# Kernel tuning notes

Hardware: AMD Instinct MI355X
Metric: run time of the kernel (lower is better)

The kernel has to match this reference:

```python
import jax, jax.numpy as jnp
import numpy as np

D_MODEL = 2048
HEADS = 16
INNER = 8192
SEQ = 2048
BATCH = 1  # source code's mask.reshape(B,1,L,L) requires B==1
EPS = 1e-5


def _layer_norm(x, gamma, beta):
    mu = jnp.mean(x, axis=-1, keepdims=True)
    var = jnp.mean(jnp.square(x - mu), axis=-1, keepdims=True)
    return (x - mu) * jax.lax.rsqrt(var + EPS) * gamma + beta


def setup_inputs() -> dict:
    key = jax.random.key(0)
    ks = jax.random.split(key, 14)
    s = 0.02
    return {
        "x": jax.random.normal(ks[0], (BATCH, SEQ, D_MODEL), jnp.float32),
        # weights stored as (in, out)
        "Wqkv": jax.random.normal(ks[1], (D_MODEL, 3 * D_MODEL), jnp.float32) * s,
        "bqkv": jnp.zeros((3 * D_MODEL,), jnp.float32),
        "Wo": jax.random.normal(ks[2], (D_MODEL, D_MODEL), jnp.float32) * s,
        "bo": jnp.zeros((D_MODEL,), jnp.float32),
        "W1": jax.random.normal(ks[3], (D_MODEL, INNER), jnp.float32) * s,
        "b1": jnp.zeros((INNER,), jnp.float32),
        "W2": jax.random.normal(ks[4], (INNER, D_MODEL), jnp.float32) * s,
        "b2": jnp.zeros((D_MODEL,), jnp.float32),
        "g1": jnp.ones((D_MODEL,), jnp.float32),
        "be1": jnp.zeros((D_MODEL,), jnp.float32),
        "g2": jnp.ones((D_MODEL,), jnp.float32),
        "be2": jnp.zeros((D_MODEL,), jnp.float32),
    }


def reference(x, Wqkv, bqkv, Wo, bo, W1, b1, W2, b2, g1, be1, g2, be2):
    B, L, D = x.shape
    H, hd = HEADS, D // HEADS
    qkv = x @ Wqkv + bqkv                       # [B,L,3D]
    q, k, v = jnp.split(qkv, 3, axis=-1)
    q = q.reshape(B, L, H, hd)
    k = k.reshape(B, L, H, hd)
    v = v.reshape(B, L, H, hd)
    # NOTE: faithful to source, scale is 1/sqrt(D) not 1/sqrt(head_dim)
    scores = jnp.einsum("bqhd,bkhd->bhqk", q, k) / jnp.sqrt(jnp.float32(D))
    causal = jnp.tril(jnp.ones((L, L), bool))   # [L,L] broadcast over B,H
    scores = jnp.where(causal, scores, -jnp.inf)
    attn = jax.nn.softmax(scores, axis=-1)      # dropout = identity (eval)
    out = jnp.einsum("bhqk,bkhd->bqhd", attn, v).reshape(B, L, D)
    lin = out @ Wo + bo
    h = _layer_norm(x + lin, g1, be1)
    ff = jax.nn.gelu(h @ W1 + b1, approximate=False) @ W2 + b2
    return _layer_norm(h + ff, g2, be2)
```

## Files before the change

kernel.cpp:

```cpp
#include <hip/hip_runtime.h>
#include <hip/hip_bf16.h>

typedef unsigned short u16;
typedef __attribute__((ext_vector_type(8))) short frag8;
typedef __attribute__((ext_vector_type(4))) float facc4;

#define L_SEQ 2048
#define D_MODEL 2048
#define N_HEADS 16
#define HEAD_D 128
#define N_QKV 6144
#define D_INNER 8192

__device__ __forceinline__ u16 f2b(float f) {
    __hip_bfloat16 h = __float2bfloat16(f);
    return *reinterpret_cast<u16*>(&h);
}

__device__ __forceinline__ float b2f(u16 u) {
    __hip_bfloat16 h = *reinterpret_cast<__hip_bfloat16*>(&u);
    return __bfloat162float(h);
}

__device__ __forceinline__ void gload_lds16(const void* g, void* l) {
    __builtin_amdgcn_global_load_lds(
        (const __attribute__((address_space(1))) unsigned int*)g,
        (__attribute__((address_space(3))) unsigned int*)l, 16, 0, 0);
}

__device__ __forceinline__ float gelu_exact(float x) {
    return 0.5f * x * (1.0f + erff(x * 0.7071067811865475f));
}

__global__ __launch_bounds__(256) void cvt_bf16_kernel(const float* __restrict__ in, u16* __restrict__ out, int n) {
    const int i = (blockIdx.x * 256 + threadIdx.x) * 8;
    if (i >= n) return;
    float4 a = *(const float4*)(in + i);
    float4 b = *(const float4*)(in + i + 4);
    u16 tmp[8];
    tmp[0] = f2b(a.x); tmp[1] = f2b(a.y); tmp[2] = f2b(a.z); tmp[3] = f2b(a.w);
    tmp[4] = f2b(b.x); tmp[5] = f2b(b.y); tmp[6] = f2b(b.z); tmp[7] = f2b(b.w);
    *(uint4*)(out + i) = *(uint4*)tmp;
}

__global__ __launch_bounds__(256) void tr_cvt64(const float* __restrict__ in, u16* __restrict__ out, int R, int C) {
    __shared__ float t[64][68];
    const int bx = blockIdx.x * 64;
    const int by = blockIdx.y * 64;
    const int tid = threadIdx.x;
    {
        const int r = tid >> 2;
        const int c4 = (tid & 3) * 16;
        const float* src = in + (size_t)(by + r) * C + bx + c4;
#pragma unroll
        for (int j = 0; j < 4; ++j)
            *(float4*)&t[r][c4 + 4 * j] = *(const float4*)(src + 4 * j);
    }
    __syncthreads();
    {
        const int cc = tid >> 2;
        const int rr0 = (tid & 3) * 16;
        u16 tmp[16];
#pragma unroll
        for (int j = 0; j < 16; ++j) tmp[j] = f2b(t[rr0 + j][cc]);
        u16* dst = out + (size_t)(bx + cc) * R + by + rr0;
        *(uint4*)(dst) = *(uint4*)&tmp[0];
        *(uint4*)(dst + 8) = *(uint4*)&tmp[8];
    }
}

template <int EPI>
__global__ __launch_bounds__(512, 2) void gemm256(const u16* __restrict__ A, const u16* __restrict__ Bt,
                                                  const float* __restrict__ bias, void* __restrict__ Cout,
                                                  u16* __restrict__ q0, u16* __restrict__ q1,
                                                  u16* __restrict__ q2, u16* __restrict__ q3,
                                                  int M, int N, int K, int kseg, int nbm) {
    __shared__ u16 lds[2 * 32768];
    const int tid = threadIdx.x;
    const int lane = tid & 63, wid = tid >> 6;
    const int wm = wid >> 2, wn = wid & 3;
    const int l15 = lane & 15, g4 = lane >> 4;

    const int nwg = gridDim.x;
    const int q8 = nwg >> 3;
    const int wg = (blockIdx.x & 7) * q8 + (blockIdx.x >> 3);
    const int bm = wg % nbm, bn = wg / nbm;
    const int kb = blockIdx.z * kseg;
    const int ksz = (blockIdx.z == (int)gridDim.z - 1) ? (K - kb) : kseg;
    const int nt = ksz >> 6;

    const int rr = tid >> 3;
    const int kk8 = tid & 7;
    const int srcE = (kk8 ^ (rr & 7)) << 3;
    const u16* aS = A + (size_t)(bm * 256 + rr) * K + kb + srcE;
    const u16* bS = Bt + (size_t)(bn * 256 + ((rr >> 5) << 6) + (rr & 31)) * K + kb + srcE;
    const size_t r128 = (size_t)128 * K;
    const size_t r64 = (size_t)64 * K;
    const size_t c32 = (size_t)32 * K;

    auto stA = [&](int tt, int h) {
        u16* d = &lds[((tt & 1) << 15) + (h << 13)];
        const u16* g = aS + (size_t)tt * 64 + (h ? r64 : 0);
        gload_lds16(g, d + tid * 8);
        gload_lds16(g + r128, d + 4096 + tid * 8);
    };
    auto stB = [&](int tt, int h) {
        u16* d = &lds[((tt & 1) << 15) + 16384 + (h << 13)];
        const u16* g = bS + (size_t)tt * 64 + (h ? c32 : 0);
        gload_lds16(g, d + tid * 8);
        gload_lds16(g + r128, d + 4096 + tid * 8);
    };

    const int ch0 = (g4 ^ (l15 & 7)) << 3;
    const int ch1 = ch0 ^ 32;
    const int aRdBase = (wm * 64 + l15) * 64;
    const int bRdBase = (wn * 32 + l15) * 64;

    frag8 a[4][2], b0[2][2], b1[2][2];
    facc4 acc[8][4] = {};

    auto rdA = [&](int bufo, int mh) {
#pragma unroll
        for (int mi = 0; mi < 4; ++mi) {
            const int base = bufo + mh * 8192 + aRdBase + mi * 1024;
            a[mi][0] = *(const frag8*)&lds[base + ch0];
            a[mi][1] = *(const frag8*)&lds[base + ch1];
        }
    };
    auto rdB = [&](int bufo, int nh, frag8(&bb)[2][2]) {
#pragma unroll
        for (int ni = 0; ni < 2; ++ni) {
            const int base = bufo + 16384 + nh * 8192 + bRdBase + ni * 1024;
            bb[ni][0] = *(const frag8*)&lds[base + ch0];
            bb[ni][1] = *(const frag8*)&lds[base + ch1];
        }
    };
    auto quad = [&](int mh, int nh, frag8(&bb)[2][2]) {
        __builtin_amdgcn_s_setprio(1);
#pragma unroll
        for (int kh = 0; kh < 2; ++kh)
#pragma unroll
            for (int mi = 0; mi < 4; ++mi)
#pragma unroll
                for (int ni = 0; ni < 2; ++ni)
                    acc[mh * 4 + mi][nh * 2 + ni] =
                        __builtin_amdgcn_mfma_f32_16x16x32_bf16(a[mi][kh], bb[ni][kh],
                                                                acc[mh * 4 + mi][nh * 2 + ni], 0, 0, 0);
        __builtin_amdgcn_s_setprio(0);
    };

#define SB __builtin_amdgcn_sched_barrier(0)
#define BAR __builtin_amdgcn_s_barrier()

    stA(0, 0); stB(0, 0); stB(0, 1); stA(0, 1);
    if (nt > 1) { stA(1, 0); stB(1, 0); stB(1, 1); }
    if (nt > 2) asm volatile("s_waitcnt vmcnt(6)" ::: "memory");
    else        asm volatile("s_waitcnt vmcnt(0)" ::: "memory");
    BAR; SB;

    for (int t = 0; t < nt; ++t) {
        const int bufo = (t & 1) << 15;
        rdA(bufo, 0);
        rdB(bufo, 0, b0);
        if (t + 1 < nt) stA(t + 1, 1);
        SB; BAR; SB;
        quad(0, 0, b0);
        BAR; SB;
        rdB(bufo, 1, b1);
        if (t + 2 < nt) stA(t + 2, 0);
        SB; BAR; SB;
        quad(0, 1, b1);
        BAR; SB;
        rdA(bufo, 1);
        if (t + 2 < nt) stB(t + 2, 0);
        SB; BAR; SB;
        quad(1, 0, b0);
        BAR; SB;
        if (t + 2 < nt) stB(t + 2, 1);
        SB; BAR; SB;
        quad(1, 1, b1);
        if (t + 2 < nt) asm volatile("s_waitcnt vmcnt(6)" ::: "memory");
        else            asm volatile("s_waitcnt vmcnt(0)" ::: "memory");
        BAR; SB;
    }
#undef SB
#undef BAR

    const int row0 = bm * 256 + wm * 128 + g4 * 4;
    const int col0 = bn * 256 + wn * 64 + l15;
    u16* pout = nullptr;
    if (EPI == 3) {
        const int z = blockIdx.z;
        pout = (z == 0) ? q0 : (z == 1) ? q1 : (z == 2) ? q2 : q3;
    }
#pragma unroll
    for (int nf = 0; nf < 4; nf++) {
        const int col = col0 + nf * 16;
        const float bv = (EPI == 3) ? 0.0f : bias[col];
#pragma unroll
        for (int mf = 0; mf < 8; mf++) {
#pragma unroll
            for (int r = 0; r < 4; r++) {
                const int row = row0 + mf * 16 + r;
                float v = acc[mf][nf][r] + bv;
                if (EPI == 2) v = gelu_exact(v);
                if (EPI == 0)
                    ((float*)Cout)[(size_t)row * N + col] = v;
                else if (EPI == 3)
                    pout[(size_t)row * N + col] = f2b(v);
                else
                    ((u16*)Cout)[(size_t)row * N + col] = f2b(v);
            }
        }
    }
}

__global__ __launch_bounds__(256) void attn_kernel(const u16* __restrict__ qkv,
                                                   float* __restrict__ O0, float* __restrict__ O1,
                                                   float* __restrict__ ml) {
    __shared__ u16 kT[2][64 * 128];
    __shared__ u16 vT[2][128 * 64];
    const int h = blockIdx.y;
    const int z = blockIdx.z;
    const int qb = (blockIdx.y < 8) ? 31 - (int)blockIdx.x : (int)blockIdx.x;
    const int tid = threadIdx.x;
    const int lane = tid & 63, w = tid >> 6;
    const int l15 = lane & 15, g4 = lane >> 4;
    const int q0 = qb * 64 + w * 16;
    const float scale = 0.022097086912079608f;

    const int ntt = qb + 1;
    const int hsp = (ntt + 1) >> 1;
    const int t0 = z ? hsp : 0;
    const int t1 = z ? ntt : hsp;

    frag8 qf[4];
    {
        const u16* qrow = qkv + (size_t)(q0 + l15) * N_QKV + h * HEAD_D + g4 * 8;
#pragma unroll
        for (int c = 0; c < 4; c++) qf[c] = *(const frag8*)(qrow + c * 32);
    }

    float m_run = -1e30f, l_run = 0.0f;
    facc4 o[8] = {};

    const int src0 = ((g4 & 1) << 5) + l15;
    const int src1 = src0 + 16;
    const bool hi = (g4 & 2) != 0;

    auto stageK = [&](int kbase, int buf) {
        const u16* kg_ptr = qkv + (size_t)kbase * N_QKV + D_MODEL + h * HEAD_D;
#pragma unroll
        for (int p = 0; p < 4; ++p) {
            const int c = p * 256 + tid;
            const int row = c >> 4;
            const int colb = (c & 15) << 4;
            const int srcb = colb ^ ((row & 7) << 4);
            gload_lds16(kg_ptr + (size_t)row * N_QKV + (srcb >> 1), &kT[buf][c * 8]);
        }
    };
    auto loadV = [&](int kbase, uint4 (&vv)[4]) {
        const u16* vg_ptr = qkv + (size_t)kbase * N_QKV + 2 * D_MODEL + h * HEAD_D;
#pragma unroll
        for (int i = 0; i < 4; ++i)
            vv[i] = *(const uint4*)(vg_ptr + (size_t)lane * N_QKV + w * 32 + i * 8);
    };
    auto writeV = [&](const uint4 (&vv)[4], int buf) {
#pragma unroll
        for (int i = 0; i < 4; ++i) {
            const u16* pv = (const u16*)&vv[i];
#pragma unroll
            for (int e = 0; e < 8; ++e) {
                const int d = w * 32 + i * 8 + e;
                vT[buf][d * 64 + ((((lane >> 3) ^ (d & 7)) << 3) | (lane & 7))] = pv[e];
            }
        }
    };

    if (t0 < t1) {
        uint4 vv[4];
        stageK(t0 * 64, 0);
        loadV(t0 * 64, vv);
        writeV(vv, 0);
    }
    __syncthreads();

    for (int t = t0; t < t1; ++t) {
        const int buf = (t - t0) & 1;
        const int kbase = t * 64;
        const bool last = (t == t1 - 1);

        uint4 vv[4];
        if (!last) {
            stageK(kbase + 64, buf ^ 1);
            loadV(kbase + 64, vv);
        }

        if (kbase <= q0 + 15) {
            const u16* kTb = kT[buf];
            const u16* vTb = vT[buf];
            float st[16];
            float mx = -1e30f;
#pragma unroll
            for (int ks = 0; ks < 4; ++ks) {
                const int k0 = kbase + ks * 16;
                if (k0 <= q0 + 15) {
                    facc4 s = {};
                    const int kl = ks * 16 + l15;
#pragma unroll
                    for (int c = 0; c < 4; ++c) {
                        const int colb = (g4 * 16 + c * 64) ^ ((kl & 7) << 4);
                        frag8 kf = *(const frag8*)&kTb[kl * 128 + (colb >> 1)];
                        s = __builtin_amdgcn_mfma_f32_16x16x32_bf16(kf, qf[c], s, 0, 0, 0);
                    }
#pragma unroll
                    for (int r = 0; r < 4; ++r) {
                        float v = s[r] * scale;
                        const int key = k0 + g4 * 4 + r;
                        if (key > q0 + l15) v = -1e30f;
                        st[ks * 4 + r] = v;
                        mx = fmaxf(mx, v);
                    }
                } else {
#pragma unroll
                    for (int r = 0; r < 4; ++r) st[ks * 4 + r] = -1e30f;
                }
            }

            mx = fmaxf(mx, __shfl_xor(mx, 16));
            mx = fmaxf(mx, __shfl_xor(mx, 32));
            const bool skip = __all(mx <= m_run + 8.0f);
            const float m_new = skip ? m_run : fmaxf(m_run, mx);
            const float alpha = __expf(m_run - m_new);
            float ps = 0.0f;
            uint2 pb[4];
#pragma unroll
            for (int ks = 0; ks < 4; ++ks) {
                const float p0 = __expf(st[ks * 4 + 0] - m_new);
                const float p1 = __expf(st[ks * 4 + 1] - m_new);
                const float p2 = __expf(st[ks * 4 + 2] - m_new);
                const float p3 = __expf(st[ks * 4 + 3] - m_new);
                ps += (p0 + p1) + (p2 + p3);
                pb[ks].x = (unsigned)f2b(p0) | ((unsigned)f2b(p1) << 16);
                pb[ks].y = (unsigned)f2b(p2) | ((unsigned)f2b(p3) << 16);
            }
            ps += __shfl_xor(ps, 16);
            ps += __shfl_xor(ps, 32);
            l_run = l_run * alpha + ps;
            m_run = m_new;
            if (!skip) {
#pragma unroll
                for (int c8 = 0; c8 < 8; ++c8)
#pragma unroll
                    for (int r = 0; r < 4; ++r) o[c8][r] *= alpha;
            }

#pragma unroll
            for (int kp = 0; kp < 2; ++kp) {
                if (kbase + kp * 32 <= q0 + 15) {
                    const uint2 a = pb[2 * kp], b = pb[2 * kp + 1];
                    const unsigned a0 = __shfl(a.x, src0), a1 = __shfl(a.y, src0);
                    const unsigned a2 = __shfl(a.x, src1), a3 = __shfl(a.y, src1);
                    const unsigned b0 = __shfl(b.x, src0), b1 = __shfl(b.y, src0);
                    const unsigned b2 = __shfl(b.x, src1), b3 = __shfl(b.y, src1);
                    union { unsigned u[4]; frag8 f; } pu;
                    pu.u[0] = hi ? b0 : a0;
                    pu.u[1] = hi ? b1 : a1;
                    pu.u[2] = hi ? b2 : a2;
                    pu.u[3] = hi ? b3 : a3;
                    const frag8 pf = pu.f;
#pragma unroll
                    for (int c8 = 0; c8 < 8; ++c8) {
                        const int d = c8 * 16 + l15;
                        const int ch = (((kp * 4 + g4) ^ (l15 & 7)) << 3);
                        frag8 vf = *(const frag8*)&vTb[d * 64 + ch];
                        o[c8] = __builtin_amdgcn_mfma_f32_16x16x32_bf16(vf, pf, o[c8], 0, 0, 0);
                    }
                }
            }
        }

        if (!last) writeV(vv, buf ^ 1);
        __syncthreads();
    }

    const int row = q0 + l15;
    if (g4 == 0) {
        const size_t mlo = (((size_t)z * N_HEADS + h) * L_SEQ + row) * 2;
        ml[mlo + 0] = m_run;
        ml[mlo + 1] = l_run;
    }
    if (t0 < t1) {
        float* Op = z ? O1 : O0;
        float* orow = Op + (size_t)row * D_MODEL + h * HEAD_D;
#pragma unroll
        for (int c8 = 0; c8 < 8; ++c8)
            *(facc4*)&orow[c8 * 16 + g4 * 4] = o[c8];
    }
}

__global__ __launch_bounds__(256) void attn_combine(const float* __restrict__ O0, const float* __restrict__ O1,
                                                    const float* __restrict__ ml, u16* __restrict__ out) {
    const int row = blockIdx.x;
    const int tid = threadIdx.x;
    const size_t rb = (size_t)row * D_MODEL;
#pragma unroll
    for (int i = 0; i < 8; ++i) {
        const int c = tid + i * 256;
        const int h = c >> 7;
        const size_t o0 = (((size_t)0 * N_HEADS + h) * L_SEQ + row) * 2;
        const size_t o1 = (((size_t)1 * N_HEADS + h) * L_SEQ + row) * 2;
        const float m0 = ml[o0 + 0], l0 = ml[o0 + 1];
        const float m1 = ml[o1 + 0], l1 = ml[o1 + 1];
        float v;
        if (l1 > 0.0f) {
            const float m = fmaxf(m0, m1);
            const float w0 = __expf(m0 - m);
            const float w1 = __expf(m1 - m);
            v = (O0[rb + c] * w0 + O1[rb + c] * w1) / (l0 * w0 + l1 * w1);
        } else {
            v = O0[rb + c] / l0;
        }
        out[rb + c] = f2b(v);
    }
}

__global__ __launch_bounds__(256) void ln1_part_kernel(const float* __restrict__ x,
                                                       const u16* __restrict__ p0, const u16* __restrict__ p1,
                                                       const u16* __restrict__ p2, const u16* __restrict__ p3,
                                                       const float* __restrict__ bias,
                                                       const float* __restrict__ gamma, const float* __restrict__ beta,
                                                       u16* __restrict__ outb) {
    __shared__ float red[8];
    const int row = blockIdx.x;
    const int tid = threadIdx.x;
    const size_t rb = (size_t)row * D_MODEL;
    float v[8];
    float s = 0.0f, s2 = 0.0f;
#pragma unroll
    for (int i = 0; i < 8; i++) {
        const int c = tid + i * 256;
        float xv = x[rb + c] + bias[c] +
                   b2f(p0[rb + c]) + b2f(p1[rb + c]) + b2f(p2[rb + c]) + b2f(p3[rb + c]);
        v[i] = xv;
        s += xv;
        s2 += xv * xv;
    }
#pragma unroll
    for (int off = 32; off; off >>= 1) {
        s += __shfl_xor(s, off);
        s2 += __shfl_xor(s2, off);
    }
    if ((tid & 63) == 0) { red[(tid >> 6) * 2] = s; red[(tid >> 6) * 2 + 1] = s2; }
    __syncthreads();
    s = red[0] + red[2] + red[4] + red[6];
    s2 = red[1] + red[3] + red[5] + red[7];
    const float mean = s * (1.0f / D_MODEL);
    const float var = s2 * (1.0f / D_MODEL) - mean * mean;
    const float rstd = rsqrtf(var + 1e-5f);
#pragma unroll
    for (int i = 0; i < 8; i++) {
        const int c = tid + i * 256;
        outb[rb + c] = f2b((v[i] - mean) * rstd * gamma[c] + beta[c]);
    }
}

__global__ __launch_bounds__(256) void ln_part_kernel(const u16* __restrict__ hb,
                                                      const u16* __restrict__ p0, const u16* __restrict__ p1,
                                                      const u16* __restrict__ p2, const u16* __restrict__ p3,
                                                      const float* __restrict__ bias,
                                                      const float* __restrict__ gamma, const float* __restrict__ beta,
                                                      float* __restrict__ outf) {
    __shared__ float red[8];
    const int row = blockIdx.x;
    const int tid = threadIdx.x;
    const size_t rb = (size_t)row * D_MODEL;
    float v[8];
    float s = 0.0f, s2 = 0.0f;
#pragma unroll
    for (int i = 0; i < 8; i++) {
        const int c = tid + i * 256;
        float x = b2f(hb[rb + c]) + bias[c] +
                  b2f(p0[rb + c]) + b2f(p1[rb + c]) + b2f(p2[rb + c]) + b2f(p3[rb + c]);
        v[i] = x;
        s += x;
        s2 += x * x;
    }
#pragma unroll
    for (int off = 32; off; off >>= 1) {
        s += __shfl_xor(s, off);
        s2 += __shfl_xor(s2, off);
    }
    if ((tid & 63) == 0) { red[(tid >> 6) * 2] = s; red[(tid >> 6) * 2 + 1] = s2; }
    __syncthreads();
    s = red[0] + red[2] + red[4] + red[6];
    s2 = red[1] + red[3] + red[5] + red[7];
    const float mean = s * (1.0f / D_MODEL);
    const float var = s2 * (1.0f / D_MODEL) - mean * mean;
    const float rstd = rsqrtf(var + 1e-5f);
#pragma unroll
    for (int i = 0; i < 8; i++) {
        const int c = tid + i * 256;
        outf[rb + c] = (v[i] - mean) * rstd * gamma[c] + beta[c];
    }
}

extern "C" void kernel_launch(void* const* d_in, const int* in_sizes, int n_in,
                              void* d_out, int out_size, void* d_ws, size_t ws_size,
                              hipStream_t stream) {
    const float* x    = (const float*)d_in[0];
    const float* Wqkv = (const float*)d_in[1];
    const float* bqkv = (const float*)d_in[2];
    const float* Wo   = (const float*)d_in[3];
    const float* bo   = (const float*)d_in[4];
    const float* W1   = (const float*)d_in[5];
    const float* b1   = (const float*)d_in[6];
    const float* W2   = (const float*)d_in[7];
    const float* b2   = (const float*)d_in[8];
    const float* g1   = (const float*)d_in[9];
    const float* be1  = (const float*)d_in[10];
    const float* g2   = (const float*)d_in[11];
    const float* be2  = (const float*)d_in[12];

    char* ws = (char*)d_ws;
    const size_t MB = 1024 * 1024;
    u16*  xb     = (u16*)(ws + 0);
    u16*  WqkvT  = (u16*)(ws + 8 * MB);
    u16*  qkv    = (u16*)(ws + 32 * MB);
    float* O0    = (float*)(ws + 0);
    float* O1    = (float*)(ws + 16 * MB);
    float* mlbuf = (float*)(ws + 56 * MB);
    u16*  attn_o = (u16*)(ws + 57 * MB);
    u16*  WoT    = (u16*)(ws + 8 * MB);
    u16*  pp0    = (u16*)(ws + 16 * MB);
    u16*  pp1    = (u16*)(ws + 24 * MB);
    u16*  pp2    = (u16*)(ws + 32 * MB);
    u16*  pp3    = (u16*)(ws + 40 * MB);
    u16*  hb     = (u16*)(ws + 0);
    u16*  W1T    = (u16*)(ws + 8 * MB);
    u16*  f1     = (u16*)(ws + 40 * MB);
    u16*  W2T    = (u16*)(ws + 72 * MB);
    u16*  part0  = (u16*)(ws + 8 * MB);
    u16*  part1  = (u16*)(ws + 16 * MB);
    u16*  part2  = (u16*)(ws + 24 * MB);
    u16*  part3  = (u16*)(ws + 32 * MB);

    cvt_bf16_kernel<<<2048, 256, 0, stream>>>(x, xb, L_SEQ * D_MODEL);
    tr_cvt64<<<dim3(N_QKV / 64, D_MODEL / 64), 256, 0, stream>>>(Wqkv, WqkvT, D_MODEL, N_QKV);
    gemm256<1><<<dim3(192, 1, 1), 512, 0, stream>>>(xb, WqkvT, bqkv, qkv, nullptr, nullptr, nullptr, nullptr,
                                                    L_SEQ, N_QKV, D_MODEL, D_MODEL, 8);
    attn_kernel<<<dim3(L_SEQ / 64, N_HEADS, 2), 256, 0, stream>>>(qkv, O0, O1, mlbuf);
    attn_combine<<<L_SEQ, 256, 0, stream>>>(O0, O1, mlbuf, attn_o);
    tr_cvt64<<<dim3(D_MODEL / 64, D_MODEL / 64), 256, 0, stream>>>(Wo, WoT, D_MODEL, D_MODEL);
    gemm256<3><<<dim3(64, 1, 4), 512, 0, stream>>>(attn_o, WoT, nullptr, nullptr, pp0, pp1, pp2, pp3,
                                                   L_SEQ, D_MODEL, D_MODEL, 512, 8);
    ln1_part_kernel<<<L_SEQ, 256, 0, stream>>>(x, pp0, pp1, pp2, pp3, bo, g1, be1, hb);
    tr_cvt64<<<dim3(D_INNER / 64, D_MODEL / 64), 256, 0, stream>>>(W1, W1T, D_MODEL, D_INNER);
    gemm256<2><<<dim3(256, 1, 1), 512, 0, stream>>>(hb, W1T, b1, f1, nullptr, nullptr, nullptr, nullptr,
                                                    L_SEQ, D_INNER, D_MODEL, D_MODEL, 8);
    tr_cvt64<<<dim3(D_MODEL / 64, D_INNER / 64), 256, 0, stream>>>(W2, W2T, D_INNER, D_MODEL);
    gemm256<3><<<dim3(64, 1, 4), 512, 0, stream>>>(f1, W2T, nullptr, nullptr, part0, part1, part2, part3,
                                                   L_SEQ, D_MODEL, D_INNER, 2048, 8);
    ln_part_kernel<<<L_SEQ, 256, 0, stream>>>(hb, part0, part1, part2, part3, b2, g2, be2, (float*)d_out);
}
```

Baseline: 458.1 us.

## Split only long-causal attention query blocks, single-buffer LDS, bf16 partials

```diff
diff --git a/kernel.cpp b/kernel.cpp
--- a/kernel.cpp
+++ b/kernel.cpp
@@ -215,14 +215,17 @@
     }
 }
 
-__global__ __launch_bounds__(256) void attn_kernel(const u16* __restrict__ qkv,
-                                                   float* __restrict__ O0, float* __restrict__ O1,
-                                                   float* __restrict__ ml) {
-    __shared__ u16 kT[2][64 * 128];
-    __shared__ u16 vT[2][128 * 64];
+__global__ __launch_bounds__(256, 4) void attn_kernel(const u16* __restrict__ qkv, u16* __restrict__ out,
+                                                      u16* __restrict__ P0, u16* __restrict__ P1,
+                                                      float* __restrict__ ml) {
+    __shared__ u16 kT[64 * 128];
+    __shared__ u16 vT[128 * 64];
     const int h = blockIdx.y;
-    const int z = blockIdx.z;
-    const int qb = (blockIdx.y < 8) ? 31 - (int)blockIdx.x : (int)blockIdx.x;
+    const int bxp = blockIdx.x;
+    int qb, z;
+    bool split;
+    if (bxp < 32) { qb = 31 - (bxp >> 1); z = bxp & 1; split = true; }
+    else          { qb = bxp - 32;        z = 0;       split = false; }
     const int tid = threadIdx.x;
     const int lane = tid & 63, w = tid >> 6;
     const int l15 = lane & 15, g4 = lane >> 4;
@@ -231,8 +234,8 @@
 
     const int ntt = qb + 1;
     const int hsp = (ntt + 1) >> 1;
-    const int t0 = z ? hsp : 0;
-    const int t1 = z ? ntt : hsp;
+    const int t0 = (split && z) ? hsp : 0;
+    const int t1 = (split && !z) ? hsp : ntt;
 
     frag8 qf[4];
     {
@@ -248,7 +251,7 @@
     const int src1 = src0 + 16;
     const bool hi = (g4 & 2) != 0;
 
-    auto stageK = [&](int kbase, int buf) {
+    auto stageK = [&](int kbase) {
         const u16* kg_ptr = qkv + (size_t)kbase * N_QKV + D_MODEL + h * HEAD_D;
 #pragma unroll
         for (int p = 0; p < 4; ++p) {
@@ -256,7 +259,7 @@
             const int row = c >> 4;
             const int colb = (c & 15) << 4;
             const int srcb = colb ^ ((row & 7) << 4);
-            gload_lds16(kg_ptr + (size_t)row * N_QKV + (srcb >> 1), &kT[buf][c * 8]);
+            gload_lds16(kg_ptr + (size_t)row * N_QKV + (srcb >> 1), &kT[c * 8]);
         }
     };
     auto loadV = [&](int kbase, uint4 (&vv)[4]) {
@@ -265,143 +268,152 @@
         for (int i = 0; i < 4; ++i)
             vv[i] = *(const uint4*)(vg_ptr + (size_t)lane * N_QKV + w * 32 + i * 8);
     };
-    auto writeV = [&](const uint4 (&vv)[4], int buf) {
+    auto writeV = [&](const uint4 (&vv)[4]) {
 #pragma unroll
         for (int i = 0; i < 4; ++i) {
             const u16* pv = (const u16*)&vv[i];
 #pragma unroll
             for (int e = 0; e < 8; ++e) {
                 const int d = w * 32 + i * 8 + e;
-                vT[buf][d * 64 + ((((lane >> 3) ^ (d & 7)) << 3) | (lane & 7))] = pv[e];
+                vT[d * 64 + ((((lane >> 3) ^ (d & 7)) << 3) | (lane & 7))] = pv[e];
             }
         }
     };
 
-    if (t0 < t1) {
+    {
         uint4 vv[4];
-        stageK(t0 * 64, 0);
+        stageK(t0 * 64);
         loadV(t0 * 64, vv);
-        writeV(vv, 0);
+        writeV(vv);
     }
     __syncthreads();
 
     for (int t = t0; t < t1; ++t) {
-        const int buf = (t - t0) & 1;
         const int kbase = t * 64;
         const bool last = (t == t1 - 1);
 
         uint4 vv[4];
-        if (!last) {
-            stageK(kbase + 64, buf ^ 1);
-            loadV(kbase + 64, vv);
-        }
-
-        if (kbase <= q0 + 15) {
-            const u16* kTb = kT[buf];
-            const u16* vTb = vT[buf];
-            float st[16];
-            float mx = -1e30f;
-#pragma unroll
-            for (int ks = 0; ks < 4; ++ks) {
-                const int k0 = kbase + ks * 16;
-                if (k0 <= q0 + 15) {
-                    facc4 s = {};
-                    const int kl = ks * 16 + l15;
-#pragma unroll
-                    for (int c = 0; c < 4; ++c) {
-                        const int colb = (g4 * 16 + c * 64) ^ ((kl & 7) << 4);
-                        frag8 kf = *(const frag8*)&kTb[kl * 128 + (colb >> 1)];
-                        s = __builtin_amdgcn_mfma_f32_16x16x32_bf16(kf, qf[c], s, 0, 0, 0);
-                    }
-#pragma unroll
-                    for (int r = 0; r < 4; ++r) {
-                        float v = s[r] * scale;
-                        const int key = k0 + g4 * 4 + r;
-                        if (key > q0 + l15) v = -1e30f;
-                        st[ks * 4 + r] = v;
-                        mx = fmaxf(mx, v);
-                    }
-                } else {
-#pragma unroll
-                    for (int r = 0; r < 4; ++r) st[ks * 4 + r] = -1e30f;
+        if (!last) loadV(kbase + 64, vv);
+
+        float st[16];
+        float mx = -1e30f;
+#pragma unroll
+        for (int ks = 0; ks < 4; ++ks) {
+            const int k0 = kbase + ks * 16;
+            if (k0 <= q0 + 15) {
+                facc4 s = {};
+                const int kl = ks * 16 + l15;
+#pragma unroll
+                for (int c = 0; c < 4; ++c) {
+                    const int colb = (g4 * 16 + c * 64) ^ ((kl & 7) << 4);
+                    frag8 kf = *(const frag8*)&kT[kl * 128 + (colb >> 1)];
+                    s = __builtin_amdgcn_mfma_f32_16x16x32_bf16(kf, qf[c], s, 0, 0, 0);
+                }
+#pragma unroll
+                for (int r = 0; r < 4; ++r) {
+                    float v = s[r] * scale;
+                    const int key = k0 + g4 * 4 + r;
+                    if (key > q0 + l15) v = -1e30f;
+                    st[ks * 4 + r] = v;
+                    mx = fmaxf(mx, v);
+                }
+            } else {
+#pragma unroll
+                for (int r = 0; r < 4; ++r) st[ks * 4 + r] = -1e30f;
+            }
+        }
+
+        mx = fmaxf(mx, __shfl_xor(mx, 16));
+        mx = fmaxf(mx, __shfl_xor(mx, 32));
+        const bool skip = __all(mx <= m_run + 8.0f);
+        const float m_new = skip ? m_run : fmaxf(m_run, mx);
+        const float alpha = __expf(m_run - m_new);
+        float ps = 0.0f;
+        uint2 pb[4];
+#pragma unroll
+        for (int ks = 0; ks < 4; ++ks) {
+            const float p0 = __expf(st[ks * 4 + 0] - m_new);
+            const float p1 = __expf(st[ks * 4 + 1] - m_new);
+            const float p2 = __expf(st[ks * 4 + 2] - m_new);
+            const float p3 = __expf(st[ks * 4 + 3] - m_new);
+            ps += (p0 + p1) + (p2 + p3);
+            pb[ks].x = (unsigned)f2b(p0) | ((unsigned)f2b(p1) << 16);
+            pb[ks].y = (unsigned)f2b(p2) | ((unsigned)f2b(p3) << 16);
+        }
+        ps += __shfl_xor(ps, 16);
+        ps += __shfl_xor(ps, 32);
+        l_run = l_run * alpha + ps;
+        m_run = m_new;
+        if (!skip) {
+#pragma unroll
+            for (int c8 = 0; c8 < 8; ++c8)
+#pragma unroll
+                for (int r = 0; r < 4; ++r) o[c8][r] *= alpha;
+        }
+
+#pragma unroll
+        for (int kp = 0; kp < 2; ++kp) {
+            if (kbase + kp * 32 <= q0 + 15) {
+                const uint2 a = pb[2 * kp], b = pb[2 * kp + 1];
+                const unsigned a0 = __shfl(a.x, src0), a1 = __shfl(a.y, src0);
+                const unsigned a2 = __shfl(a.x, src1), a3 = __shfl(a.y, src1);
+                const unsigned b0 = __shfl(b.x, src0), b1 = __shfl(b.y, src0);
+                const unsigned b2 = __shfl(b.x, src1), b3 = __shfl(b.y, src1);
+                union { unsigned u[4]; frag8 f; } pu;
+                pu.u[0] = hi ? b0 : a0;
+                pu.u[1] = hi ? b1 : a1;
+                pu.u[2] = hi ? b2 : a2;
+                pu.u[3] = hi ? b3 : a3;
+                const frag8 pf = pu.f;
+#pragma unroll
+                for (int c8 = 0; c8 < 8; ++c8) {
+                    const int d = c8 * 16 + l15;
+                    const int ch = (((kp * 4 + g4) ^ (l15 & 7)) << 3);
+                    frag8 vf = *(const frag8*)&vT[d * 64 + ch];
+                    o[c8] = __builtin_amdgcn_mfma_f32_16x16x32_bf16(vf, pf, o[c8], 0, 0, 0);
                 }
             }
-
-            mx = fmaxf(mx, __shfl_xor(mx, 16));
-            mx = fmaxf(mx, __shfl_xor(mx, 32));
-            const bool skip = __all(mx <= m_run + 8.0f);
-            const float m_new = skip ? m_run : fmaxf(m_run, mx);
-            const float alpha = __expf(m_run - m_new);
-            float ps = 0.0f;
-            uint2 pb[4];
-#pragma unroll
-            for (int ks = 0; ks < 4; ++ks) {
-                const float p0 = __expf(st[ks * 4 + 0] - m_new);
-                const float p1 = __expf(st[ks * 4 + 1] - m_new);
-                const float p2 = __expf(st[ks * 4 + 2] - m_new);
-                const float p3 = __expf(st[ks * 4 + 3] - m_new);
-                ps += (p0 + p1) + (p2 + p3);
-                pb[ks].x = (unsigned)f2b(p0) | ((unsigned)f2b(p1) << 16);
-                pb[ks].y = (unsigned)f2b(p2) | ((unsigned)f2b(p3) << 16);
-            }
-            ps += __shfl_xor(ps, 16);
-            ps += __shfl_xor(ps, 32);
-            l_run = l_run * alpha + ps;
-            m_run = m_new;
-            if (!skip) {
-#pragma unroll
-                for (int c8 = 0; c8 < 8; ++c8)
-#pragma unroll
-                    for (int r = 0; r < 4; ++r) o[c8][r] *= alpha;
-            }
-
-#pragma unroll
-            for (int kp = 0; kp < 2; ++kp) {
-                if (kbase + kp * 32 <= q0 + 15) {
-                    const uint2 a = pb[2 * kp], b = pb[2 * kp + 1];
-                    const unsigned a0 = __shfl(a.x, src0), a1 = __shfl(a.y, src0);
-                    const unsigned a2 = __shfl(a.x, src1), a3 = __shfl(a.y, src1);
-                    const unsigned b0 = __shfl(b.x, src0), b1 = __shfl(b.y, src0);
-                    const unsigned b2 = __shfl(b.x, src1), b3 = __shfl(b.y, src1);
-                    union { unsigned u[4]; frag8 f; } pu;
-                    pu.u[0] = hi ? b0 : a0;
-                    pu.u[1] = hi ? b1 : a1;
-                    pu.u[2] = hi ? b2 : a2;
-                    pu.u[3] = hi ? b3 : a3;
-                    const frag8 pf = pu.f;
-#pragma unroll
-                    for (int c8 = 0; c8 < 8; ++c8) {
-                        const int d = c8 * 16 + l15;
-                        const int ch = (((kp * 4 + g4) ^ (l15 & 7)) << 3);
-                        frag8 vf = *(const frag8*)&vTb[d * 64 + ch];
-                        o[c8] = __builtin_amdgcn_mfma_f32_16x16x32_bf16(vf, pf, o[c8], 0, 0, 0);
-                    }
-                }
-            }
-        }
-
-        if (!last) writeV(vv, buf ^ 1);
-        __syncthreads();
+        }
+
+        if (!last) {
+            __syncthreads();
+            stageK(kbase + 64);
+            writeV(vv);
+            __syncthreads();
+        }
     }
 
     const int row = q0 + l15;
-    if (g4 == 0) {
-        const size_t mlo = (((size_t)z * N_HEADS + h) * L_SEQ + row) * 2;
-        ml[mlo + 0] = m_run;
-        ml[mlo + 1] = l_run;
-    }
-    if (t0 < t1) {
-        float* Op = z ? O1 : O0;
-        float* orow = Op + (size_t)row * D_MODEL + h * HEAD_D;
-#pragma unroll
-        for (int c8 = 0; c8 < 8; ++c8)
-            *(facc4*)&orow[c8 * 16 + g4 * 4] = o[c8];
-    }
-}
-
-__global__ __launch_bounds__(256) void attn_combine(const float* __restrict__ O0, const float* __restrict__ O1,
+    if (!split) {
+        const float inv_l = 1.0f / l_run;
+        u16* orow = out + (size_t)row * D_MODEL + h * HEAD_D;
+#pragma unroll
+        for (int c8 = 0; c8 < 8; ++c8) {
+            uint2 st2;
+            st2.x = (unsigned)f2b(o[c8][0] * inv_l) | ((unsigned)f2b(o[c8][1] * inv_l) << 16);
+            st2.y = (unsigned)f2b(o[c8][2] * inv_l) | ((unsigned)f2b(o[c8][3] * inv_l) << 16);
+            *(uint2*)&orow[c8 * 16 + g4 * 4] = st2;
+        }
+    } else {
+        if (g4 == 0) {
+            const size_t mlo = (((size_t)z * N_HEADS + h) * L_SEQ + row) * 2;
+            ml[mlo + 0] = m_run;
+            ml[mlo + 1] = l_run;
+        }
+        u16* prow = (z ? P1 : P0) + (size_t)row * D_MODEL + h * HEAD_D;
+#pragma unroll
+        for (int c8 = 0; c8 < 8; ++c8) {
+            uint2 st2;
+            st2.x = (unsigned)f2b(o[c8][0]) | ((unsigned)f2b(o[c8][1]) << 16);
+            st2.y = (unsigned)f2b(o[c8][2]) | ((unsigned)f2b(o[c8][3]) << 16);
+            *(uint2*)&prow[c8 * 16 + g4 * 4] = st2;
+        }
+    }
+}
+
+__global__ __launch_bounds__(256) void attn_combine(const u16* __restrict__ P0, const u16* __restrict__ P1,
                                                     const float* __restrict__ ml, u16* __restrict__ out) {
-    const int row = blockIdx.x;
+    const int row = 1024 + blockIdx.x;
     const int tid = threadIdx.x;
     const size_t rb = (size_t)row * D_MODEL;
 #pragma unroll
@@ -412,15 +424,10 @@
         const size_t o1 = (((size_t)1 * N_HEADS + h) * L_SEQ + row) * 2;
         const float m0 = ml[o0 + 0], l0 = ml[o0 + 1];
         const float m1 = ml[o1 + 0], l1 = ml[o1 + 1];
-        float v;
-        if (l1 > 0.0f) {
-            const float m = fmaxf(m0, m1);
-            const float w0 = __expf(m0 - m);
-            const float w1 = __expf(m1 - m);
-            v = (O0[rb + c] * w0 + O1[rb + c] * w1) / (l0 * w0 + l1 * w1);
-        } else {
-            v = O0[rb + c] / l0;
-        }
+        const float m = fmaxf(m0, m1);
+        const float w0 = __expf(m0 - m);
+        const float w1 = __expf(m1 - m);
+        const float v = (b2f(P0[rb + c]) * w0 + b2f(P1[rb + c]) * w1) / (l0 * w0 + l1 * w1);
         out[rb + c] = f2b(v);
     }
 }
@@ -527,8 +534,8 @@
     u16*  xb     = (u16*)(ws + 0);
     u16*  WqkvT  = (u16*)(ws + 8 * MB);
     u16*  qkv    = (u16*)(ws + 32 * MB);
-    float* O0    = (float*)(ws + 0);
-    float* O1    = (float*)(ws + 16 * MB);
+    u16*  P0     = (u16*)(ws + 0);
+    u16*  P1     = (u16*)(ws + 8 * MB);
     float* mlbuf = (float*)(ws + 56 * MB);
     u16*  attn_o = (u16*)(ws + 57 * MB);
     u16*  WoT    = (u16*)(ws + 8 * MB);
@@ -549,8 +556,8 @@
     tr_cvt64<<<dim3(N_QKV / 64, D_MODEL / 64), 256, 0, stream>>>(Wqkv, WqkvT, D_MODEL, N_QKV);
     gemm256<1><<<dim3(192, 1, 1), 512, 0, stream>>>(xb, WqkvT, bqkv, qkv, nullptr, nullptr, nullptr, nullptr,
                                                     L_SEQ, N_QKV, D_MODEL, D_MODEL, 8);
-    attn_kernel<<<dim3(L_SEQ / 64, N_HEADS, 2), 256, 0, stream>>>(qkv, O0, O1, mlbuf);
-    attn_combine<<<L_SEQ, 256, 0, stream>>>(O0, O1, mlbuf, attn_o);
+    attn_kernel<<<dim3(48, N_HEADS), 256, 0, stream>>>(qkv, attn_o, P0, P1, mlbuf);
+    attn_combine<<<1024, 256, 0, stream>>>(P0, P1, mlbuf, attn_o);
     tr_cvt64<<<dim3(D_MODEL / 64, D_MODEL / 64), 256, 0, stream>>>(Wo, WoT, D_MODEL, D_MODEL);
     gemm256<3><<<dim3(64, 1, 4), 512, 0, stream>>>(attn_o, WoT, nullptr, nullptr, pp0, pp1, pp2, pp3,
                                                    L_SEQ, D_MODEL, D_MODEL, 512, 8);
```

Measured after the change: 469.7 us. +2.5%, slower.
